# Kernel optimization log

Measured on AMD Instinct MI355X. Metric: run time of the kernel, lower is better.

The kernel has to match this reference:

```python
import jax, jax.numpy as jnp
import numpy as np

N_NODES = 100000
N_EDGES = 1600000
NUM_RELS = 200
NUM_BASES = 4
IN_FEAT = 20   # hardcoded by `view(-1, 1, 20)` in the torch source
OUT_FEAT = 20
SUBMAT_IN = IN_FEAT // NUM_BASES   # 5
SUBMAT_OUT = OUT_FEAT // NUM_BASES # 5


def setup_inputs() -> dict:
    key = jax.random.key(0)
    ks = jax.random.split(key, 9)
    return {
        "h": jax.random.normal(ks[0], (N_NODES, IN_FEAT), dtype=jnp.float32),
        "weight": jax.random.normal(ks[1], (NUM_RELS, NUM_BASES * SUBMAT_IN * SUBMAT_OUT), dtype=jnp.float32),
        "bias_term": jax.random.normal(ks[2], (NUM_RELS, OUT_FEAT), dtype=jnp.float32),
        "gate_weight": jax.random.normal(ks[3], (NUM_RELS, OUT_FEAT, 1), dtype=jnp.float32),
        "gate_bias": jax.random.normal(ks[4], (NUM_RELS, 1), dtype=jnp.float32),
        "loop_weight": jax.random.normal(ks[5], (IN_FEAT, OUT_FEAT), dtype=jnp.float32),
        "edge_src": jax.random.randint(ks[6], (N_EDGES,), 0, N_NODES, dtype=jnp.int32),
        "edge_dst": jax.random.randint(ks[7], (N_EDGES,), 0, N_NODES, dtype=jnp.int32),
        "etype": jax.random.randint(ks[8], (NUM_RELS,), 0, NUM_RELS, dtype=jnp.int32) if False else jax.random.randint(ks[8], (N_EDGES,), 0, NUM_RELS, dtype=jnp.int32),
    }


def reference(h, weight, bias_term, gate_weight, gate_bias, loop_weight, edge_src, edge_dst, etype):
    n_nodes = h.shape[0]
    # self-loop message (dropout=0.0 -> identity)
    loop_message = h @ loop_weight                                    # [N, out]
    # per-edge relation-indexed gathers
    W = weight[etype].reshape(-1, NUM_BASES, SUBMAT_IN, SUBMAT_OUT)   # [E, B, si, so]
    src = h[edge_src]                                                 # [E, in]
    node = src.reshape(-1, NUM_BASES, SUBMAT_IN)                      # [E, B, si]
    # block-diagonal small matmul
    msg = jnp.einsum('ebi,ebio->ebo', node, W).reshape(-1, OUT_FEAT)  # [E, out]
    # gate: sigmoid(<full src node, gate_weight_r> + gate_bias_r)
    gw = gate_weight[etype, :, 0]                                     # [E, out(=20=in)]
    gb = gate_bias[etype, 0]                                          # [E]
    gate = jax.nn.sigmoid(jnp.sum(src * gw, axis=-1) + gb)            # [E]
    msg = gate[:, None] * (msg + bias_term[etype])                    # [E, out]
    # scatter-sum aggregation to destination nodes (zero init for isolated nodes)
    agg = jax.ops.segment_sum(msg, edge_dst, num_segments=n_nodes)    # [N, out]
    return jax.nn.relu(agg + loop_message)
```

## Files before the change

kernel.cpp:

```cpp
#include <hip/hip_runtime.h>
#include <hip/hip_fp16.h>
#include <math.h>

#define IN_FEAT 20
#define OUT_FEAT 20
#define NUM_BASES 4
#define SUBMAT_IN 5
#define SUBMAT_OUT 5
#define NUM_RELS 200
#define CAP 64
#define NPB 160
#define BCAP 3072


__global__ void zero_kernel(int* __restrict__ p, int n) {
    int i = blockIdx.x * blockDim.x + threadIdx.x;
    if (i < n) p[i] = 0;
}

__global__ void __launch_bounds__(1024)
bucket_scatter_kernel(const int* __restrict__ edge_src,
                      const int* __restrict__ edge_dst,
                      const int* __restrict__ etype,
                      int* __restrict__ cursor,
                      int2* __restrict__ bucketed,
                      int n_edges, int nb) {
    __shared__ int lhist[1024];
    __shared__ int lbase[1024];
    __shared__ int lrank[1024];
    int tid = threadIdx.x;
    for (int i = tid; i < nb; i += 1024) { lhist[i] = 0; lrank[i] = 0; }
    __syncthreads();

    int e0 = blockIdx.x * 4096 + tid * 4;
    int s[4], d[4], t[4], bk[4];
    bool val[4];
    if (e0 + 3 < n_edges) {
        int4 sv = *(const int4*)(edge_src + e0);
        int4 dv = *(const int4*)(edge_dst + e0);
        int4 tv = *(const int4*)(etype + e0);
        s[0]=sv.x; s[1]=sv.y; s[2]=sv.z; s[3]=sv.w;
        d[0]=dv.x; d[1]=dv.y; d[2]=dv.z; d[3]=dv.w;
        t[0]=tv.x; t[1]=tv.y; t[2]=tv.z; t[3]=tv.w;
        val[0]=val[1]=val[2]=val[3]=true;
    } else {
#pragma unroll
        for (int k = 0; k < 4; ++k) {
            int e = e0 + k;
            val[k] = (e < n_edges);
            s[k] = val[k] ? edge_src[e] : 0;
            d[k] = val[k] ? edge_dst[e] : 0;
            t[k] = val[k] ? etype[e] : 0;
        }
    }
#pragma unroll
    for (int k = 0; k < 4; ++k) {
        bk[k] = d[k] / NPB;
        if (val[k]) atomicAdd(&lhist[bk[k]], 1);
    }
    __syncthreads();
    for (int i = tid; i < nb; i += 1024)
        if (lhist[i] > 0) lbase[i] = atomicAdd(&cursor[i], lhist[i]);
    __syncthreads();
#pragma unroll
    for (int k = 0; k < 4; ++k) {
        if (val[k]) {
            int r = atomicAdd(&lrank[bk[k]], 1);
            int off = lbase[bk[k]] + r;
            if (off < BCAP) {
                unsigned packed = (unsigned)s[k] | ((unsigned)t[k] << 17);
                bucketed[(size_t)bk[k] * BCAP + off] = make_int2(d[k], (int)packed);
            }
        }
    }
}

__global__ void __launch_bounds__(1024)
bucket_scan_kernel(const int* __restrict__ cursor, int* __restrict__ bucket_base,
                   int nb) {
    __shared__ int s[1024];
    int tid = threadIdx.x;
    int v = (tid < nb) ? min(cursor[tid], BCAP) : 0;
    s[tid] = v;
    __syncthreads();
    for (int step = 1; step < 1024; step <<= 1) {
        int t = (tid >= step) ? s[tid - step] : 0;
        __syncthreads();
        if (tid >= step) s[tid] += t;
        __syncthreads();
    }
    if (tid < nb) bucket_base[tid] = s[tid] - v;
}

__global__ void __launch_bounds__(1024)
place_csr_kernel(const int* __restrict__ cursor,
                 const int* __restrict__ bucket_base,
                 const int2* __restrict__ bucketed,
                 unsigned* __restrict__ records,
                 int* __restrict__ cnt,
                 int* __restrict__ off,
                 int n_nodes) {
    __shared__ int lcnt[NPB];
    __shared__ int sscan[NPB];
    __shared__ int lrank[NPB];
    int b = blockIdx.x, tid = threadIdx.x;
    int node0 = b * NPB;
    if (tid < NPB) { lcnt[tid] = 0; lrank[tid] = 0; }
    __syncthreads();
    int m = cursor[b]; if (m > BCAP) m = BCAP;
    int gbase = bucket_base[b];

    for (int i = tid; i < m; i += 1024) {
        int2 r = bucketed[(size_t)b * BCAP + i];
        atomicAdd(&lcnt[r.x - node0], 1);
    }
    __syncthreads();
    if (tid < NPB) sscan[tid] = lcnt[tid];
    __syncthreads();
    for (int step = 1; step < NPB; step <<= 1) {
        int t = (tid < NPB && tid >= step) ? sscan[tid - step] : 0;
        __syncthreads();
        if (tid < NPB && tid >= step) sscan[tid] += t;
        __syncthreads();
    }
    if (tid < NPB) {
        int excl = sscan[tid] - lcnt[tid];
        int v = node0 + tid;
        if (v < n_nodes) { cnt[v] = lcnt[tid]; off[v] = gbase + excl; }
        sscan[tid] = excl;
    }
    __syncthreads();
    for (int i = tid; i < m; i += 1024) {
        int2 r = bucketed[(size_t)b * BCAP + i];
        int dl = r.x - node0;
        int rk = atomicAdd(&lrank[dl], 1);
        records[(size_t)gbase + sscan[dl] + rk] = (unsigned)r.y;
    }
}

__global__ void __launch_bounds__(256)
hpad_kernel(const float* __restrict__ h, __half* __restrict__ h_pad, int n_nodes) {
    int v = blockIdx.x * 256 + threadIdx.x;
    if (v >= n_nodes) return;
    const float4* hp = (const float4*)(h + (size_t)v * IN_FEAT);
    float4 a = hp[0], b = hp[1], c = hp[2], d = hp[3], e = hp[4];
    __half2 p0 = __floats2half2_rn(a.x, a.y), p1 = __floats2half2_rn(a.z, a.w);
    __half2 p2 = __floats2half2_rn(b.x, b.y), p3 = __floats2half2_rn(b.z, b.w);
    __half2 p4 = __floats2half2_rn(c.x, c.y), p5 = __floats2half2_rn(c.z, c.w);
    __half2 p6 = __floats2half2_rn(d.x, d.y), p7 = __floats2half2_rn(d.z, d.w);
    __half2 p8 = __floats2half2_rn(e.x, e.y), p9 = __floats2half2_rn(e.z, e.w);
    uint4 w0, w1; uint2 w2;
    w0.x = *(unsigned*)&p0; w0.y = *(unsigned*)&p1; w0.z = *(unsigned*)&p2; w0.w = *(unsigned*)&p3;
    w1.x = *(unsigned*)&p4; w1.y = *(unsigned*)&p5; w1.z = *(unsigned*)&p6; w1.w = *(unsigned*)&p7;
    w2.x = *(unsigned*)&p8; w2.y = *(unsigned*)&p9;
    char* dst = (char*)(h_pad + (size_t)v * 32);
    *(uint4*)(dst)      = w0;
    *(uint4*)(dst + 16) = w1;
    *(uint2*)(dst + 32) = w2;
}

__global__ void __launch_bounds__(1024, 4)
gather_kernel(const float* __restrict__ h,
              const __half* __restrict__ h_pad,
              const float* __restrict__ loop_weight,
              const float* __restrict__ weight,
              const float* __restrict__ bias_term,
              const float* __restrict__ gate_weight,
              const float* __restrict__ gate_bias,
              const int* __restrict__ cnt,
              const int* __restrict__ off,
              const unsigned* __restrict__ records,
              float* __restrict__ out, int n_nodes, int n_groups) {
    __shared__ __half2 lds_wp[NUM_RELS * 51];
    __shared__ float   lds_gwt[IN_FEAT * NUM_RELS];
    __shared__ float   lds_gb[NUM_RELS];
    __shared__ float   lds_lw[IN_FEAT * OUT_FEAT];
    int tid = threadIdx.x;
    for (int idx = tid; idx < NUM_RELS * 50; idx += 1024) {
        int t = idx / 50, f = idx - t * 50;
        lds_wp[t * 51 + f] = __floats2half2_rn(weight[t * 100 + f],
                                               weight[t * 100 + f + 50]);
    }
    for (int idx = tid; idx < IN_FEAT * NUM_RELS; idx += 1024) {
        int t = idx / IN_FEAT, i = idx - t * IN_FEAT;
        lds_gwt[i * NUM_RELS + t] = gate_weight[idx];
    }
    for (int idx = tid; idx < NUM_RELS; idx += 1024) lds_gb[idx] = gate_bias[idx];
    for (int idx = tid; idx < IN_FEAT * OUT_FEAT; idx += 1024) lds_lw[idx] = loop_weight[idx];
    __syncthreads();

    int wave = blockIdx.x * 16 + (tid >> 6);
    int nwaves = gridDim.x * 16;
    int l = tid & 63;
    int l16 = l & 15;

    for (int grp = wave; grp < n_groups; grp += nwaves) {
        int v = grp * 4 + (l >> 4);
        bool valid = (v < n_nodes);
        int c = 0, base = 0;
        if (valid) { c = cnt[v]; base = off[v]; }
        if (c > CAP) c = CAP;

        float acc[OUT_FEAT];
#pragma unroll
        for (int j = 0; j < OUT_FEAT; ++j) acc[j] = 0.0f;

        if (valid) {
#pragma unroll
            for (int i0 = 0; i0 < 2; ++i0) {
                int i = l16 + i0 * 16;
                if (i < IN_FEAT) {
                    float s = h[(size_t)v * IN_FEAT + i];
#pragma unroll
                    for (int j = 0; j < OUT_FEAT; ++j)
                        acc[j] = fmaf(s, lds_lw[i * OUT_FEAT + j], acc[j]);
                }
            }
        }

#pragma unroll
        for (int it = 0; it < 4; ++it) {
            int slot = l16 + it * 16;
            if (valid && slot < c) {
                unsigned p = records[(size_t)base + slot];
                int srcid = (int)(p & 0x1FFFFu);
                int t = (int)(p >> 17);

                const char* sp = (const char*)(h_pad + (size_t)srcid * 32);
                uint4 A = *(const uint4*)(sp);
                uint4 B = *(const uint4*)(sp + 16);
                uint2 C = *(const uint2*)(sp + 32);
                float src[IN_FEAT];
                {
                    unsigned u[10] = {A.x, A.y, A.z, A.w, B.x, B.y, B.z, B.w, C.x, C.y};
#pragma unroll
                    for (int q = 0; q < 10; ++q) {
                        __half2 hv = *reinterpret_cast<__half2*>(&u[q]);
                        float2 f = __half22float2(hv);
                        src[2 * q] = f.x; src[2 * q + 1] = f.y;
                    }
                }

                float g = lds_gb[t];
#pragma unroll
                for (int i = 0; i < IN_FEAT; ++i)
                    g = fmaf(src[i], lds_gwt[i * NUM_RELS + t], g);
                g = 1.0f / (1.0f + __expf(-g));

#pragma unroll
                for (int i = 0; i < IN_FEAT; ++i) src[i] *= g;

                const __half2* wp = lds_wp + t * 51;
#pragma unroll
                for (int f = 0; f < 50; ++f) {
                    float2 w = __half22float2(wp[f]);
                    const int b0 = f / 25, r = f - b0 * 25;
                    const int i0 = r / 5, o0 = r - i0 * 5;
                    acc[b0 * 5 + o0] =
                        fmaf(src[b0 * 5 + i0], w.x, acc[b0 * 5 + o0]);
                    acc[(b0 + 2) * 5 + o0] =
                        fmaf(src[(b0 + 2) * 5 + i0], w.y, acc[(b0 + 2) * 5 + o0]);
                }

                const float4* btp = (const float4*)(bias_term + (size_t)t * OUT_FEAT);
#pragma unroll
                for (int k = 0; k < OUT_FEAT / 4; ++k) {
                    float4 bv = btp[k];
                    acc[4 * k + 0] = fmaf(g, bv.x, acc[4 * k + 0]);
                    acc[4 * k + 1] = fmaf(g, bv.y, acc[4 * k + 1]);
                    acc[4 * k + 2] = fmaf(g, bv.z, acc[4 * k + 2]);
                    acc[4 * k + 3] = fmaf(g, bv.w, acc[4 * k + 3]);
                }
            }
        }

#pragma unroll
        for (int mask = 8; mask > 0; mask >>= 1) {
#pragma unroll
            for (int j = 0; j < OUT_FEAT; ++j)
                acc[j] += __shfl_xor(acc[j], mask, 16);
        }

        if (valid && l16 < OUT_FEAT / 4) {
            float4 tv;
            tv.x = fmaxf(acc[4 * l16 + 0], 0.0f);
            tv.y = fmaxf(acc[4 * l16 + 1], 0.0f);
            tv.z = fmaxf(acc[4 * l16 + 2], 0.0f);
            tv.w = fmaxf(acc[4 * l16 + 3], 0.0f);
            ((float4*)(out + (size_t)v * OUT_FEAT))[l16] = tv;
        }
    }
}

__global__ void loop_msg_kernel(const float* __restrict__ h,
                                const float* __restrict__ loop_weight,
                                float* __restrict__ out, int n_nodes) {
    int v = blockIdx.x * blockDim.x + threadIdx.x;
    if (v >= n_nodes) return;
    float src[IN_FEAT];
    const float4* hp = (const float4*)(h + (size_t)v * IN_FEAT);
#pragma unroll
    for (int i = 0; i < IN_FEAT / 4; ++i) {
        float4 t = hp[i];
        src[4 * i + 0] = t.x; src[4 * i + 1] = t.y;
        src[4 * i + 2] = t.z; src[4 * i + 3] = t.w;
    }
    float acc[OUT_FEAT];
#pragma unroll
    for (int j = 0; j < OUT_FEAT; ++j) acc[j] = 0.0f;
#pragma unroll
    for (int i = 0; i < IN_FEAT; ++i) {
        float s = src[i];
#pragma unroll
        for (int j = 0; j < OUT_FEAT; ++j)
            acc[j] = fmaf(s, loop_weight[i * OUT_FEAT + j], acc[j]);
    }
    float4* op = (float4*)(out + (size_t)v * OUT_FEAT);
#pragma unroll
    for (int j = 0; j < OUT_FEAT / 4; ++j) {
        float4 t;
        t.x = acc[4 * j + 0]; t.y = acc[4 * j + 1];
        t.z = acc[4 * j + 2]; t.w = acc[4 * j + 3];
        op[j] = t;
    }
}

__global__ void edge_atomic_kernel(const float* __restrict__ h,
                                   const float* __restrict__ weight,
                                   const float* __restrict__ bias_term,
                                   const float* __restrict__ gate_weight,
                                   const float* __restrict__ gate_bias,
                                   const int* __restrict__ edge_src,
                                   const int* __restrict__ edge_dst,
                                   const int* __restrict__ etype,
                                   float* __restrict__ out, int n_edges) {
    int e = blockIdx.x * blockDim.x + threadIdx.x;
    if (e >= n_edges) return;
    int s = edge_src[e], d = edge_dst[e], t = etype[e];
    float src[IN_FEAT];
    const float4* hp = (const float4*)(h + (size_t)s * IN_FEAT);
#pragma unroll
    for (int i = 0; i < IN_FEAT / 4; ++i) {
        float4 v = hp[i];
        src[4 * i + 0] = v.x; src[4 * i + 1] = v.y;
        src[4 * i + 2] = v.z; src[4 * i + 3] = v.w;
    }
    const float* W = weight + (size_t)t * 100;
    float msg[OUT_FEAT];
#pragma unroll
    for (int j = 0; j < OUT_FEAT; ++j) msg[j] = 0.0f;
#pragma unroll
    for (int b = 0; b < NUM_BASES; ++b)
#pragma unroll
        for (int i = 0; i < SUBMAT_IN; ++i) {
            float sv = src[b * SUBMAT_IN + i];
#pragma unroll
            for (int o = 0; o < SUBMAT_OUT; ++o)
                msg[b * SUBMAT_OUT + o] =
                    fmaf(sv, W[(b * SUBMAT_IN + i) * SUBMAT_OUT + o],
                         msg[b * SUBMAT_OUT + o]);
        }
    const float* gw = gate_weight + (size_t)t * OUT_FEAT;
    float g = gate_bias[t];
#pragma unroll
    for (int i = 0; i < IN_FEAT; ++i) g = fmaf(src[i], gw[i], g);
    g = 1.0f / (1.0f + __expf(-g));
    const float* bt = bias_term + (size_t)t * OUT_FEAT;
    float* dstp = out + (size_t)d * OUT_FEAT;
#pragma unroll
    for (int j = 0; j < OUT_FEAT; ++j) atomicAdd(&dstp[j], g * (msg[j] + bt[j]));
}

__global__ void relu_kernel(float* __restrict__ out, int n4) {
    int i = blockIdx.x * blockDim.x + threadIdx.x;
    if (i >= n4) return;
    float4* p = (float4*)out;
    float4 v = p[i];
    v.x = fmaxf(v.x, 0.0f); v.y = fmaxf(v.y, 0.0f);
    v.z = fmaxf(v.z, 0.0f); v.w = fmaxf(v.w, 0.0f);
    p[i] = v;
}

extern "C" void kernel_launch(void* const* d_in, const int* in_sizes, int n_in,
                              void* d_out, int out_size, void* d_ws, size_t ws_size,
                              hipStream_t stream) {
    const float* h           = (const float*)d_in[0];
    const float* weight      = (const float*)d_in[1];
    const float* bias_term   = (const float*)d_in[2];
    const float* gate_weight = (const float*)d_in[3];
    const float* gate_bias   = (const float*)d_in[4];
    const float* loop_weight = (const float*)d_in[5];
    const int* edge_src      = (const int*)d_in[6];
    const int* edge_dst      = (const int*)d_in[7];
    const int* etype         = (const int*)d_in[8];
    float* out = (float*)d_out;

    const int n_nodes = in_sizes[0] / IN_FEAT;
    const int n_edges = in_sizes[6];
    const int nb = (n_nodes + NPB - 1) / NPB;

    size_t off_cursor   = 0;
    size_t off_bbase    = (((size_t)nb * 4 + 127) / 128) * 128;
    size_t off_bucketed = ((off_bbase + (size_t)nb * 4 + 127) / 128) * 128;
    size_t off_records  = ((off_bucketed + (size_t)nb * BCAP * 8 + 127) / 128) * 128;
    size_t off_cnt      = ((off_records + (size_t)n_edges * 4 + 127) / 128) * 128;
    size_t off_offs     = ((off_cnt + (size_t)n_nodes * 4 + 127) / 128) * 128;
    size_t off_hpad     = ((off_offs + (size_t)n_nodes * 4 + 127) / 128) * 128;
    size_t need = off_hpad + (size_t)n_nodes * 64;

    bool ok = (ws_size >= need) && (n_nodes <= (1 << 17)) && (nb <= 1024) &&
              (in_sizes[4] == NUM_RELS) && (in_sizes[1] == NUM_RELS * 100) &&
              (in_sizes[5] == IN_FEAT * OUT_FEAT);

    if (ok) {
        int*  cursor      = (int*)((char*)d_ws + off_cursor);
        int*  bucket_base = (int*)((char*)d_ws + off_bbase);
        int2* bucketed    = (int2*)((char*)d_ws + off_bucketed);
        unsigned* records = (unsigned*)((char*)d_ws + off_records);
        int*  cnt         = (int*)((char*)d_ws + off_cnt);
        int*  off         = (int*)((char*)d_ws + off_offs);
        __half* h_pad     = (__half*)((char*)d_ws + off_hpad);

        zero_kernel<<<(nb + 255) / 256, 256, 0, stream>>>(cursor, nb);
        hpad_kernel<<<(n_nodes + 255) / 256, 256, 0, stream>>>(h, h_pad, n_nodes);
        bucket_scatter_kernel<<<(n_edges + 4095) / 4096, 1024, 0, stream>>>(
            edge_src, edge_dst, etype, cursor, bucketed, n_edges, nb);
        bucket_scan_kernel<<<1, 1024, 0, stream>>>(cursor, bucket_base, nb);
        place_csr_kernel<<<nb, 1024, 0, stream>>>(
            cursor, bucket_base, bucketed, records, cnt, off, n_nodes);
        int n_groups = (n_nodes + 3) / 4;
        gather_kernel<<<512, 1024, 0, stream>>>(
            h, h_pad, loop_weight, weight, bias_term, gate_weight, gate_bias,
            cnt, off, records, out, n_nodes, n_groups);
    } else {
        loop_msg_kernel<<<(n_nodes + 255) / 256, 256, 0, stream>>>(
            h, loop_weight, out, n_nodes);
        edge_atomic_kernel<<<(n_edges + 255) / 256, 256, 0, stream>>>(
            h, weight, bias_term, gate_weight, gate_bias,
            edge_src, edge_dst, etype, out, n_edges);
        relu_kernel<<<(n_nodes * OUT_FEAT / 4 + 255) / 256, 256, 0, stream>>>(
            out, n_nodes * OUT_FEAT / 4);
    }
}
```

Baseline: 205.9 us.

## Aggregate directly from destination buckets with LDS atomics, dropping CSR build

Removes the scan and CSR placement kernels and replaces the per-node gather with a per-bucket aggregation kernel. Each block processes one destination bucket's edges, accumulates messages into shared memory with float atomics, then adds the self-loop matmul and applies ReLU. It also folds cursor zeroing into the h_pad conversion kernel. This cuts two launches and the records/cnt/off traffic, at the cost of LDS atomic contention, nondeterministic summation order, and re-staging the relation tables in shared memory once per bucket block (about 625 blocks instead of 512).

```diff
diff --git a/kernel.cpp b/kernel.cpp
--- a/kernel.cpp
+++ b/kernel.cpp
@@ -8,139 +8,16 @@
 #define SUBMAT_IN 5
 #define SUBMAT_OUT 5
 #define NUM_RELS 200
-#define CAP 64
 #define NPB 160
 #define BCAP 3072
-
-
-__global__ void zero_kernel(int* __restrict__ p, int n) {
-    int i = blockIdx.x * blockDim.x + threadIdx.x;
-    if (i < n) p[i] = 0;
-}
-
-__global__ void __launch_bounds__(1024)
-bucket_scatter_kernel(const int* __restrict__ edge_src,
-                      const int* __restrict__ edge_dst,
-                      const int* __restrict__ etype,
-                      int* __restrict__ cursor,
-                      int2* __restrict__ bucketed,
-                      int n_edges, int nb) {
-    __shared__ int lhist[1024];
-    __shared__ int lbase[1024];
-    __shared__ int lrank[1024];
-    int tid = threadIdx.x;
-    for (int i = tid; i < nb; i += 1024) { lhist[i] = 0; lrank[i] = 0; }
-    __syncthreads();
-
-    int e0 = blockIdx.x * 4096 + tid * 4;
-    int s[4], d[4], t[4], bk[4];
-    bool val[4];
-    if (e0 + 3 < n_edges) {
-        int4 sv = *(const int4*)(edge_src + e0);
-        int4 dv = *(const int4*)(edge_dst + e0);
-        int4 tv = *(const int4*)(etype + e0);
-        s[0]=sv.x; s[1]=sv.y; s[2]=sv.z; s[3]=sv.w;
-        d[0]=dv.x; d[1]=dv.y; d[2]=dv.z; d[3]=dv.w;
-        t[0]=tv.x; t[1]=tv.y; t[2]=tv.z; t[3]=tv.w;
-        val[0]=val[1]=val[2]=val[3]=true;
-    } else {
-#pragma unroll
-        for (int k = 0; k < 4; ++k) {
-            int e = e0 + k;
-            val[k] = (e < n_edges);
-            s[k] = val[k] ? edge_src[e] : 0;
-            d[k] = val[k] ? edge_dst[e] : 0;
-            t[k] = val[k] ? etype[e] : 0;
-        }
-    }
-#pragma unroll
-    for (int k = 0; k < 4; ++k) {
-        bk[k] = d[k] / NPB;
-        if (val[k]) atomicAdd(&lhist[bk[k]], 1);
-    }
-    __syncthreads();
-    for (int i = tid; i < nb; i += 1024)
-        if (lhist[i] > 0) lbase[i] = atomicAdd(&cursor[i], lhist[i]);
-    __syncthreads();
-#pragma unroll
-    for (int k = 0; k < 4; ++k) {
-        if (val[k]) {
-            int r = atomicAdd(&lrank[bk[k]], 1);
-            int off = lbase[bk[k]] + r;
-            if (off < BCAP) {
-                unsigned packed = (unsigned)s[k] | ((unsigned)t[k] << 17);
-                bucketed[(size_t)bk[k] * BCAP + off] = make_int2(d[k], (int)packed);
-            }
-        }
-    }
-}
-
-__global__ void __launch_bounds__(1024)
-bucket_scan_kernel(const int* __restrict__ cursor, int* __restrict__ bucket_base,
-                   int nb) {
-    __shared__ int s[1024];
-    int tid = threadIdx.x;
-    int v = (tid < nb) ? min(cursor[tid], BCAP) : 0;
-    s[tid] = v;
-    __syncthreads();
-    for (int step = 1; step < 1024; step <<= 1) {
-        int t = (tid >= step) ? s[tid - step] : 0;
-        __syncthreads();
-        if (tid >= step) s[tid] += t;
-        __syncthreads();
-    }
-    if (tid < nb) bucket_base[tid] = s[tid] - v;
-}
-
-__global__ void __launch_bounds__(1024)
-place_csr_kernel(const int* __restrict__ cursor,
-                 const int* __restrict__ bucket_base,
-                 const int2* __restrict__ bucketed,
-                 unsigned* __restrict__ records,
-                 int* __restrict__ cnt,
-                 int* __restrict__ off,
-                 int n_nodes) {
-    __shared__ int lcnt[NPB];
-    __shared__ int sscan[NPB];
-    __shared__ int lrank[NPB];
-    int b = blockIdx.x, tid = threadIdx.x;
-    int node0 = b * NPB;
-    if (tid < NPB) { lcnt[tid] = 0; lrank[tid] = 0; }
-    __syncthreads();
-    int m = cursor[b]; if (m > BCAP) m = BCAP;
-    int gbase = bucket_base[b];
-
-    for (int i = tid; i < m; i += 1024) {
-        int2 r = bucketed[(size_t)b * BCAP + i];
-        atomicAdd(&lcnt[r.x - node0], 1);
-    }
-    __syncthreads();
-    if (tid < NPB) sscan[tid] = lcnt[tid];
-    __syncthreads();
-    for (int step = 1; step < NPB; step <<= 1) {
-        int t = (tid < NPB && tid >= step) ? sscan[tid - step] : 0;
-        __syncthreads();
-        if (tid < NPB && tid >= step) sscan[tid] += t;
-        __syncthreads();
-    }
-    if (tid < NPB) {
-        int excl = sscan[tid] - lcnt[tid];
-        int v = node0 + tid;
-        if (v < n_nodes) { cnt[v] = lcnt[tid]; off[v] = gbase + excl; }
-        sscan[tid] = excl;
-    }
-    __syncthreads();
-    for (int i = tid; i < m; i += 1024) {
-        int2 r = bucketed[(size_t)b * BCAP + i];
-        int dl = r.x - node0;
-        int rk = atomicAdd(&lrank[dl], 1);
-        records[(size_t)gbase + sscan[dl] + rk] = (unsigned)r.y;
-    }
-}
+#define ACCW 21
+
 
 __global__ void __launch_bounds__(256)
-hpad_kernel(const float* __restrict__ h, __half* __restrict__ h_pad, int n_nodes) {
+hpad_zero_kernel(const float* __restrict__ h, __half* __restrict__ h_pad,
+                 int* __restrict__ cursor, int n_nodes, int nb) {
     int v = blockIdx.x * 256 + threadIdx.x;
+    if (v < nb) cursor[v] = 0;
     if (v >= n_nodes) return;
     const float4* hp = (const float4*)(h + (size_t)v * IN_FEAT);
     float4 a = hp[0], b = hp[1], c = hp[2], d = hp[3], e = hp[4];
@@ -159,23 +36,83 @@
     *(uint2*)(dst + 32) = w2;
 }
 
+__global__ void __launch_bounds__(1024)
+bucket_scatter_kernel(const int* __restrict__ edge_src,
+                      const int* __restrict__ edge_dst,
+                      const int* __restrict__ etype,
+                      int* __restrict__ cursor,
+                      int2* __restrict__ bucketed,
+                      int n_edges, int nb) {
+    __shared__ int lhist[1024];
+    __shared__ int lbase[1024];
+    __shared__ int lrank[1024];
+    int tid = threadIdx.x;
+    for (int i = tid; i < nb; i += 1024) { lhist[i] = 0; lrank[i] = 0; }
+    __syncthreads();
+
+    int e0 = blockIdx.x * 4096 + tid * 4;
+    int s[4], d[4], t[4], bk[4];
+    bool val[4];
+    if (e0 + 3 < n_edges) {
+        int4 sv = *(const int4*)(edge_src + e0);
+        int4 dv = *(const int4*)(edge_dst + e0);
+        int4 tv = *(const int4*)(etype + e0);
+        s[0]=sv.x; s[1]=sv.y; s[2]=sv.z; s[3]=sv.w;
+        d[0]=dv.x; d[1]=dv.y; d[2]=dv.z; d[3]=dv.w;
+        t[0]=tv.x; t[1]=tv.y; t[2]=tv.z; t[3]=tv.w;
+        val[0]=val[1]=val[2]=val[3]=true;
+    } else {
+#pragma unroll
+        for (int k = 0; k < 4; ++k) {
+            int e = e0 + k;
+            val[k] = (e < n_edges);
+            s[k] = val[k] ? edge_src[e] : 0;
+            d[k] = val[k] ? edge_dst[e] : 0;
+            t[k] = val[k] ? etype[e] : 0;
+        }
+    }
+#pragma unroll
+    for (int k = 0; k < 4; ++k) {
+        bk[k] = d[k] / NPB;
+        if (val[k]) atomicAdd(&lhist[bk[k]], 1);
+    }
+    __syncthreads();
+    for (int i = tid; i < nb; i += 1024)
+        if (lhist[i] > 0) lbase[i] = atomicAdd(&cursor[i], lhist[i]);
+    __syncthreads();
+#pragma unroll
+    for (int k = 0; k < 4; ++k) {
+        if (val[k]) {
+            int r = atomicAdd(&lrank[bk[k]], 1);
+            int off = lbase[bk[k]] + r;
+            if (off < BCAP) {
+                unsigned packed = (unsigned)s[k] | ((unsigned)t[k] << 17);
+                bucketed[(size_t)bk[k] * BCAP + off] = make_int2(d[k], (int)packed);
+            }
+        }
+    }
+}
+
 __global__ void __launch_bounds__(1024, 4)
-gather_kernel(const float* __restrict__ h,
-              const __half* __restrict__ h_pad,
-              const float* __restrict__ loop_weight,
-              const float* __restrict__ weight,
-              const float* __restrict__ bias_term,
-              const float* __restrict__ gate_weight,
-              const float* __restrict__ gate_bias,
-              const int* __restrict__ cnt,
-              const int* __restrict__ off,
-              const unsigned* __restrict__ records,
-              float* __restrict__ out, int n_nodes, int n_groups) {
+bucket_aggregate_kernel(const float* __restrict__ h,
+                        const __half* __restrict__ h_pad,
+                        const float* __restrict__ loop_weight,
+                        const float* __restrict__ weight,
+                        const float* __restrict__ bias_term,
+                        const float* __restrict__ gate_weight,
+                        const float* __restrict__ gate_bias,
+                        const int* __restrict__ cursor,
+                        const int2* __restrict__ bucketed,
+                        float* __restrict__ out, int n_nodes) {
     __shared__ __half2 lds_wp[NUM_RELS * 51];
     __shared__ float   lds_gwt[IN_FEAT * NUM_RELS];
     __shared__ float   lds_gb[NUM_RELS];
     __shared__ float   lds_lw[IN_FEAT * OUT_FEAT];
+    __shared__ float   lds_acc[NPB * ACCW];
     int tid = threadIdx.x;
+    int b = blockIdx.x;
+    int node0 = b * NPB;
+
     for (int idx = tid; idx < NUM_RELS * 50; idx += 1024) {
         int t = idx / 50, f = idx - t * 50;
         lds_wp[t * 51 + f] = __floats2half2_rn(weight[t * 100 + f],
@@ -187,107 +124,79 @@
     }
     for (int idx = tid; idx < NUM_RELS; idx += 1024) lds_gb[idx] = gate_bias[idx];
     for (int idx = tid; idx < IN_FEAT * OUT_FEAT; idx += 1024) lds_lw[idx] = loop_weight[idx];
-    __syncthreads();
-
-    int wave = blockIdx.x * 16 + (tid >> 6);
-    int nwaves = gridDim.x * 16;
-    int l = tid & 63;
-    int l16 = l & 15;
-
-    for (int grp = wave; grp < n_groups; grp += nwaves) {
-        int v = grp * 4 + (l >> 4);
-        bool valid = (v < n_nodes);
-        int c = 0, base = 0;
-        if (valid) { c = cnt[v]; base = off[v]; }
-        if (c > CAP) c = CAP;
-
-        float acc[OUT_FEAT];
-#pragma unroll
-        for (int j = 0; j < OUT_FEAT; ++j) acc[j] = 0.0f;
-
-        if (valid) {
-#pragma unroll
-            for (int i0 = 0; i0 < 2; ++i0) {
-                int i = l16 + i0 * 16;
-                if (i < IN_FEAT) {
-                    float s = h[(size_t)v * IN_FEAT + i];
-#pragma unroll
-                    for (int j = 0; j < OUT_FEAT; ++j)
-                        acc[j] = fmaf(s, lds_lw[i * OUT_FEAT + j], acc[j]);
-                }
-            }
-        }
-
-#pragma unroll
-        for (int it = 0; it < 4; ++it) {
-            int slot = l16 + it * 16;
-            if (valid && slot < c) {
-                unsigned p = records[(size_t)base + slot];
-                int srcid = (int)(p & 0x1FFFFu);
-                int t = (int)(p >> 17);
-
-                const char* sp = (const char*)(h_pad + (size_t)srcid * 32);
-                uint4 A = *(const uint4*)(sp);
-                uint4 B = *(const uint4*)(sp + 16);
-                uint2 C = *(const uint2*)(sp + 32);
-                float src[IN_FEAT];
-                {
-                    unsigned u[10] = {A.x, A.y, A.z, A.w, B.x, B.y, B.z, B.w, C.x, C.y};
-#pragma unroll
-                    for (int q = 0; q < 10; ++q) {
-                        __half2 hv = *reinterpret_cast<__half2*>(&u[q]);
-                        float2 f = __half22float2(hv);
-                        src[2 * q] = f.x; src[2 * q + 1] = f.y;
-                    }
-                }
-
-                float g = lds_gb[t];
-#pragma unroll
-                for (int i = 0; i < IN_FEAT; ++i)
-                    g = fmaf(src[i], lds_gwt[i * NUM_RELS + t], g);
-                g = 1.0f / (1.0f + __expf(-g));
-
-#pragma unroll
-                for (int i = 0; i < IN_FEAT; ++i) src[i] *= g;
-
-                const __half2* wp = lds_wp + t * 51;
-#pragma unroll
-                for (int f = 0; f < 50; ++f) {
-                    float2 w = __half22float2(wp[f]);
-                    const int b0 = f / 25, r = f - b0 * 25;
-                    const int i0 = r / 5, o0 = r - i0 * 5;
-                    acc[b0 * 5 + o0] =
-                        fmaf(src[b0 * 5 + i0], w.x, acc[b0 * 5 + o0]);
-                    acc[(b0 + 2) * 5 + o0] =
-                        fmaf(src[(b0 + 2) * 5 + i0], w.y, acc[(b0 + 2) * 5 + o0]);
-                }
-
-                const float4* btp = (const float4*)(bias_term + (size_t)t * OUT_FEAT);
-#pragma unroll
-                for (int k = 0; k < OUT_FEAT / 4; ++k) {
-                    float4 bv = btp[k];
-                    acc[4 * k + 0] = fmaf(g, bv.x, acc[4 * k + 0]);
-                    acc[4 * k + 1] = fmaf(g, bv.y, acc[4 * k + 1]);
-                    acc[4 * k + 2] = fmaf(g, bv.z, acc[4 * k + 2]);
-                    acc[4 * k + 3] = fmaf(g, bv.w, acc[4 * k + 3]);
-                }
-            }
-        }
-
-#pragma unroll
-        for (int mask = 8; mask > 0; mask >>= 1) {
-#pragma unroll
-            for (int j = 0; j < OUT_FEAT; ++j)
-                acc[j] += __shfl_xor(acc[j], mask, 16);
-        }
-
-        if (valid && l16 < OUT_FEAT / 4) {
-            float4 tv;
-            tv.x = fmaxf(acc[4 * l16 + 0], 0.0f);
-            tv.y = fmaxf(acc[4 * l16 + 1], 0.0f);
-            tv.z = fmaxf(acc[4 * l16 + 2], 0.0f);
-            tv.w = fmaxf(acc[4 * l16 + 3], 0.0f);
-            ((float4*)(out + (size_t)v * OUT_FEAT))[l16] = tv;
+    for (int idx = tid; idx < NPB * ACCW; idx += 1024) lds_acc[idx] = 0.0f;
+    __syncthreads();
+
+    int m = cursor[b]; if (m > BCAP) m = BCAP;
+
+    for (int i = tid; i < m; i += 1024) {
+        int2 r = bucketed[(size_t)b * BCAP + i];
+        int dl = r.x - node0;
+        unsigned p = (unsigned)r.y;
+        int srcid = (int)(p & 0x1FFFFu);
+        int t = (int)(p >> 17);
+
+        const char* sp = (const char*)(h_pad + (size_t)srcid * 32);
+        uint4 A = *(const uint4*)(sp);
+        uint4 B = *(const uint4*)(sp + 16);
+        uint2 C = *(const uint2*)(sp + 32);
+        float src[IN_FEAT];
+        {
+            unsigned u0;
+            float2 f2;
+#define UNP(word, o) u0 = (word); f2 = __half22float2(*reinterpret_cast<__half2*>(&u0)); \
+                     src[(o)] = f2.x; src[(o) + 1] = f2.y;
+            UNP(A.x, 0)  UNP(A.y, 2)  UNP(A.z, 4)  UNP(A.w, 6)
+            UNP(B.x, 8)  UNP(B.y, 10) UNP(B.z, 12) UNP(B.w, 14)
+            UNP(C.x, 16) UNP(C.y, 18)
+#undef UNP
+        }
+
+        float g = lds_gb[t];
+#pragma unroll
+        for (int i2 = 0; i2 < IN_FEAT; ++i2)
+            g = fmaf(src[i2], lds_gwt[i2 * NUM_RELS + t], g);
+        g = 1.0f / (1.0f + __expf(-g));
+
+#pragma unroll
+        for (int i2 = 0; i2 < IN_FEAT; ++i2) src[i2] *= g;
+
+        float msg[OUT_FEAT];
+        const float4* btp = (const float4*)(bias_term + (size_t)t * OUT_FEAT);
+#pragma unroll
+        for (int k = 0; k < OUT_FEAT / 4; ++k) {
+            float4 bv = btp[k];
+            msg[4 * k + 0] = g * bv.x; msg[4 * k + 1] = g * bv.y;
+            msg[4 * k + 2] = g * bv.z; msg[4 * k + 3] = g * bv.w;
+        }
+
+        const __half2* wp = lds_wp + t * 51;
+#pragma unroll
+        for (int f = 0; f < 50; ++f) {
+            float2 w = __half22float2(wp[f]);
+            const int b0 = f / 25, rr = f - b0 * 25;
+            const int i0 = rr / 5, o0 = rr - i0 * 5;
+            msg[b0 * 5 + o0] = fmaf(src[b0 * 5 + i0], w.x, msg[b0 * 5 + o0]);
+            msg[(b0 + 2) * 5 + o0] = fmaf(src[(b0 + 2) * 5 + i0], w.y, msg[(b0 + 2) * 5 + o0]);
+        }
+
+        float* accp = lds_acc + dl * ACCW;
+#pragma unroll
+        for (int j = 0; j < OUT_FEAT; ++j)
+            atomicAdd(&accp[j], msg[j]);
+    }
+    __syncthreads();
+
+    for (int task = tid; task < NPB * OUT_FEAT; task += 1024) {
+        int vl = task / OUT_FEAT, j = task - vl * OUT_FEAT;
+        int v = node0 + vl;
+        if (v < n_nodes) {
+            const float* hv = h + (size_t)v * IN_FEAT;
+            float s = lds_acc[vl * ACCW + j];
+#pragma unroll
+            for (int i2 = 0; i2 < IN_FEAT; ++i2)
+                s = fmaf(hv[i2], lds_lw[i2 * OUT_FEAT + j], s);
+            out[(size_t)v * OUT_FEAT + j] = fmaxf(s, 0.0f);
         }
     }
 }
@@ -400,12 +309,8 @@
     const int nb = (n_nodes + NPB - 1) / NPB;
 
     size_t off_cursor   = 0;
-    size_t off_bbase    = (((size_t)nb * 4 + 127) / 128) * 128;
-    size_t off_bucketed = ((off_bbase + (size_t)nb * 4 + 127) / 128) * 128;
-    size_t off_records  = ((off_bucketed + (size_t)nb * BCAP * 8 + 127) / 128) * 128;
-    size_t off_cnt      = ((off_records + (size_t)n_edges * 4 + 127) / 128) * 128;
-    size_t off_offs     = ((off_cnt + (size_t)n_nodes * 4 + 127) / 128) * 128;
-    size_t off_hpad     = ((off_offs + (size_t)n_nodes * 4 + 127) / 128) * 128;
+    size_t off_bucketed = (((size_t)nb * 4 + 127) / 128) * 128;
+    size_t off_hpad     = ((off_bucketed + (size_t)nb * BCAP * 8 + 127) / 128) * 128;
     size_t need = off_hpad + (size_t)n_nodes * 64;
 
     bool ok = (ws_size >= need) && (n_nodes <= (1 << 17)) && (nb <= 1024) &&
@@ -414,24 +319,16 @@
 
     if (ok) {
         int*  cursor      = (int*)((char*)d_ws + off_cursor);
-        int*  bucket_base = (int*)((char*)d_ws + off_bbase);
         int2* bucketed    = (int2*)((char*)d_ws + off_bucketed);
-        unsigned* records = (unsigned*)((char*)d_ws + off_records);
-        int*  cnt         = (int*)((char*)d_ws + off_cnt);
-        int*  off         = (int*)((char*)d_ws + off_offs);
         __half* h_pad     = (__half*)((char*)d_ws + off_hpad);
 
-        zero_kernel<<<(nb + 255) / 256, 256, 0, stream>>>(cursor, nb);
-        hpad_kernel<<<(n_nodes + 255) / 256, 256, 0, stream>>>(h, h_pad, n_nodes);
+        hpad_zero_kernel<<<(n_nodes + 255) / 256, 256, 0, stream>>>(
+            h, h_pad, cursor, n_nodes, nb);
         bucket_scatter_kernel<<<(n_edges + 4095) / 4096, 1024, 0, stream>>>(
             edge_src, edge_dst, etype, cursor, bucketed, n_edges, nb);
-        bucket_scan_kernel<<<1, 1024, 0, stream>>>(cursor, bucket_base, nb);
-        place_csr_kernel<<<nb, 1024, 0, stream>>>(
-            cursor, bucket_base, bucketed, records, cnt, off, n_nodes);
-        int n_groups = (n_nodes + 3) / 4;
-        gather_kernel<<<512, 1024, 0, stream>>>(
+        bucket_aggregate_kernel<<<nb, 1024, 0, stream>>>(
             h, h_pad, loop_weight, weight, bias_term, gate_weight, gate_bias,
-            cnt, off, records, out, n_nodes, n_groups);
+            cursor, bucketed, out, n_nodes);
     } else {
         loop_msg_kernel<<<(n_nodes + 255) / 256, 256, 0, stream>>>(
             h, loop_weight, out, n_nodes);
```

Measured after the change: 347.5 us. 68.7% more time.

## Fuse CSR placement into gather kernel using per-bucket LDS records

Applied to the files above, without the earlier changes.

Removes the global bucket scan and place_csr kernels. Each gather block now owns one bucket of 160 destination nodes: it counts and scans edges in LDS, places the records in LDS, and then aggregates. The zero-init is also folded into the hpad kernel. This drops two launches and a global round trip of the records, cnt and off arrays. In exchange every one of the ~625 blocks reloads the relation weight tables into LDS and uses more shared memory, which may lower occupancy.

```diff
diff --git a/kernel.cpp b/kernel.cpp
--- a/kernel.cpp
+++ b/kernel.cpp
@@ -11,136 +11,14 @@
 #define CAP 64
 #define NPB 160
 #define BCAP 3072
-
-
-__global__ void zero_kernel(int* __restrict__ p, int n) {
-    int i = blockIdx.x * blockDim.x + threadIdx.x;
-    if (i < n) p[i] = 0;
-}
-
-__global__ void __launch_bounds__(1024)
-bucket_scatter_kernel(const int* __restrict__ edge_src,
-                      const int* __restrict__ edge_dst,
-                      const int* __restrict__ etype,
-                      int* __restrict__ cursor,
-                      int2* __restrict__ bucketed,
-                      int n_edges, int nb) {
-    __shared__ int lhist[1024];
-    __shared__ int lbase[1024];
-    __shared__ int lrank[1024];
-    int tid = threadIdx.x;
-    for (int i = tid; i < nb; i += 1024) { lhist[i] = 0; lrank[i] = 0; }
-    __syncthreads();
-
-    int e0 = blockIdx.x * 4096 + tid * 4;
-    int s[4], d[4], t[4], bk[4];
-    bool val[4];
-    if (e0 + 3 < n_edges) {
-        int4 sv = *(const int4*)(edge_src + e0);
-        int4 dv = *(const int4*)(edge_dst + e0);
-        int4 tv = *(const int4*)(etype + e0);
-        s[0]=sv.x; s[1]=sv.y; s[2]=sv.z; s[3]=sv.w;
-        d[0]=dv.x; d[1]=dv.y; d[2]=dv.z; d[3]=dv.w;
-        t[0]=tv.x; t[1]=tv.y; t[2]=tv.z; t[3]=tv.w;
-        val[0]=val[1]=val[2]=val[3]=true;
-    } else {
-#pragma unroll
-        for (int k = 0; k < 4; ++k) {
-            int e = e0 + k;
-            val[k] = (e < n_edges);
-            s[k] = val[k] ? edge_src[e] : 0;
-            d[k] = val[k] ? edge_dst[e] : 0;
-            t[k] = val[k] ? etype[e] : 0;
-        }
-    }
-#pragma unroll
-    for (int k = 0; k < 4; ++k) {
-        bk[k] = d[k] / NPB;
-        if (val[k]) atomicAdd(&lhist[bk[k]], 1);
-    }
-    __syncthreads();
-    for (int i = tid; i < nb; i += 1024)
-        if (lhist[i] > 0) lbase[i] = atomicAdd(&cursor[i], lhist[i]);
-    __syncthreads();
-#pragma unroll
-    for (int k = 0; k < 4; ++k) {
-        if (val[k]) {
-            int r = atomicAdd(&lrank[bk[k]], 1);
-            int off = lbase[bk[k]] + r;
-            if (off < BCAP) {
-                unsigned packed = (unsigned)s[k] | ((unsigned)t[k] << 17);
-                bucketed[(size_t)bk[k] * BCAP + off] = make_int2(d[k], (int)packed);
-            }
-        }
-    }
-}
-
-__global__ void __launch_bounds__(1024)
-bucket_scan_kernel(const int* __restrict__ cursor, int* __restrict__ bucket_base,
-                   int nb) {
-    __shared__ int s[1024];
-    int tid = threadIdx.x;
-    int v = (tid < nb) ? min(cursor[tid], BCAP) : 0;
-    s[tid] = v;
-    __syncthreads();
-    for (int step = 1; step < 1024; step <<= 1) {
-        int t = (tid >= step) ? s[tid - step] : 0;
-        __syncthreads();
-        if (tid >= step) s[tid] += t;
-        __syncthreads();
-    }
-    if (tid < nb) bucket_base[tid] = s[tid] - v;
-}
-
-__global__ void __launch_bounds__(1024)
-place_csr_kernel(const int* __restrict__ cursor,
-                 const int* __restrict__ bucket_base,
-                 const int2* __restrict__ bucketed,
-                 unsigned* __restrict__ records,
-                 int* __restrict__ cnt,
-                 int* __restrict__ off,
-                 int n_nodes) {
-    __shared__ int lcnt[NPB];
-    __shared__ int sscan[NPB];
-    __shared__ int lrank[NPB];
-    int b = blockIdx.x, tid = threadIdx.x;
-    int node0 = b * NPB;
-    if (tid < NPB) { lcnt[tid] = 0; lrank[tid] = 0; }
-    __syncthreads();
-    int m = cursor[b]; if (m > BCAP) m = BCAP;
-    int gbase = bucket_base[b];
-
-    for (int i = tid; i < m; i += 1024) {
-        int2 r = bucketed[(size_t)b * BCAP + i];
-        atomicAdd(&lcnt[r.x - node0], 1);
-    }
-    __syncthreads();
-    if (tid < NPB) sscan[tid] = lcnt[tid];
-    __syncthreads();
-    for (int step = 1; step < NPB; step <<= 1) {
-        int t = (tid < NPB && tid >= step) ? sscan[tid - step] : 0;
-        __syncthreads();
-        if (tid < NPB && tid >= step) sscan[tid] += t;
-        __syncthreads();
-    }
-    if (tid < NPB) {
-        int excl = sscan[tid] - lcnt[tid];
-        int v = node0 + tid;
-        if (v < n_nodes) { cnt[v] = lcnt[tid]; off[v] = gbase + excl; }
-        sscan[tid] = excl;
-    }
-    __syncthreads();
-    for (int i = tid; i < m; i += 1024) {
-        int2 r = bucketed[(size_t)b * BCAP + i];
-        int dl = r.x - node0;
-        int rk = atomicAdd(&lrank[dl], 1);
-        records[(size_t)gbase + sscan[dl] + rk] = (unsigned)r.y;
-    }
-}
+#define NPASS ((NPB + 63) / 64)
+
 
 __global__ void __launch_bounds__(256)
-hpad_kernel(const float* __restrict__ h, __half* __restrict__ h_pad, int n_nodes) {
+hpad_zero_kernel(const float* __restrict__ h, __half* __restrict__ h_pad,
+                 int* __restrict__ cursor, int n_nodes, int nb) {
     int v = blockIdx.x * 256 + threadIdx.x;
+    if (v < nb) cursor[v] = 0;
     if (v >= n_nodes) return;
     const float4* hp = (const float4*)(h + (size_t)v * IN_FEAT);
     float4 a = hp[0], b = hp[1], c = hp[2], d = hp[3], e = hp[4];
@@ -159,23 +37,86 @@
     *(uint2*)(dst + 32) = w2;
 }
 
+__global__ void __launch_bounds__(1024)
+bucket_scatter_kernel(const int* __restrict__ edge_src,
+                      const int* __restrict__ edge_dst,
+                      const int* __restrict__ etype,
+                      int* __restrict__ cursor,
+                      int2* __restrict__ bucketed,
+                      int n_edges, int nb) {
+    __shared__ int lhist[1024];
+    __shared__ int lbase[1024];
+    __shared__ int lrank[1024];
+    int tid = threadIdx.x;
+    for (int i = tid; i < nb; i += 1024) { lhist[i] = 0; lrank[i] = 0; }
+    __syncthreads();
+
+    int e0 = blockIdx.x * 4096 + tid * 4;
+    int s[4], d[4], t[4], bk[4];
+    bool val[4];
+    if (e0 + 3 < n_edges) {
+        int4 sv = *(const int4*)(edge_src + e0);
+        int4 dv = *(const int4*)(edge_dst + e0);
+        int4 tv = *(const int4*)(etype + e0);
+        s[0]=sv.x; s[1]=sv.y; s[2]=sv.z; s[3]=sv.w;
+        d[0]=dv.x; d[1]=dv.y; d[2]=dv.z; d[3]=dv.w;
+        t[0]=tv.x; t[1]=tv.y; t[2]=tv.z; t[3]=tv.w;
+        val[0]=val[1]=val[2]=val[3]=true;
+    } else {
+#pragma unroll
+        for (int k = 0; k < 4; ++k) {
+            int e = e0 + k;
+            val[k] = (e < n_edges);
+            s[k] = val[k] ? edge_src[e] : 0;
+            d[k] = val[k] ? edge_dst[e] : 0;
+            t[k] = val[k] ? etype[e] : 0;
+        }
+    }
+#pragma unroll
+    for (int k = 0; k < 4; ++k) {
+        bk[k] = d[k] / NPB;
+        if (val[k]) atomicAdd(&lhist[bk[k]], 1);
+    }
+    __syncthreads();
+    for (int i = tid; i < nb; i += 1024)
+        if (lhist[i] > 0) lbase[i] = atomicAdd(&cursor[i], lhist[i]);
+    __syncthreads();
+#pragma unroll
+    for (int k = 0; k < 4; ++k) {
+        if (val[k]) {
+            int r = atomicAdd(&lrank[bk[k]], 1);
+            int off = lbase[bk[k]] + r;
+            if (off < BCAP) {
+                unsigned packed = (unsigned)s[k] | ((unsigned)t[k] << 17);
+                bucketed[(size_t)bk[k] * BCAP + off] = make_int2(d[k], (int)packed);
+            }
+        }
+    }
+}
+
 __global__ void __launch_bounds__(1024, 4)
-gather_kernel(const float* __restrict__ h,
-              const __half* __restrict__ h_pad,
-              const float* __restrict__ loop_weight,
-              const float* __restrict__ weight,
-              const float* __restrict__ bias_term,
-              const float* __restrict__ gate_weight,
-              const float* __restrict__ gate_bias,
-              const int* __restrict__ cnt,
-              const int* __restrict__ off,
-              const unsigned* __restrict__ records,
-              float* __restrict__ out, int n_nodes, int n_groups) {
-    __shared__ __half2 lds_wp[NUM_RELS * 51];
-    __shared__ float   lds_gwt[IN_FEAT * NUM_RELS];
-    __shared__ float   lds_gb[NUM_RELS];
-    __shared__ float   lds_lw[IN_FEAT * OUT_FEAT];
+bucket_gather_kernel(const float* __restrict__ h,
+                     const __half* __restrict__ h_pad,
+                     const float* __restrict__ loop_weight,
+                     const float* __restrict__ weight,
+                     const float* __restrict__ bias_term,
+                     const float* __restrict__ gate_weight,
+                     const float* __restrict__ gate_bias,
+                     const int* __restrict__ cursor,
+                     const int2* __restrict__ bucketed,
+                     float* __restrict__ out, int n_nodes) {
+    __shared__ __half2  lds_wp[NUM_RELS * 51];
+    __shared__ float    lds_gwt[IN_FEAT * NUM_RELS];
+    __shared__ float    lds_gb[NUM_RELS];
+    __shared__ float    lds_lw[IN_FEAT * OUT_FEAT];
+    __shared__ unsigned lds_rec[BCAP];
+    __shared__ int      lcnt[NPB];
+    __shared__ int      loff[NPB];
+    __shared__ int      lrank[NPB];
     int tid = threadIdx.x;
+    int b = blockIdx.x;
+    int node0 = b * NPB;
+
     for (int idx = tid; idx < NUM_RELS * 50; idx += 1024) {
         int t = idx / 50, f = idx - t * 50;
         lds_wp[t * 51 + f] = __floats2half2_rn(weight[t * 100 + f],
@@ -187,19 +128,47 @@
     }
     for (int idx = tid; idx < NUM_RELS; idx += 1024) lds_gb[idx] = gate_bias[idx];
     for (int idx = tid; idx < IN_FEAT * OUT_FEAT; idx += 1024) lds_lw[idx] = loop_weight[idx];
-    __syncthreads();
-
-    int wave = blockIdx.x * 16 + (tid >> 6);
-    int nwaves = gridDim.x * 16;
+    if (tid < NPB) { lcnt[tid] = 0; lrank[tid] = 0; }
+    __syncthreads();
+
+    int m = cursor[b]; if (m > BCAP) m = BCAP;
+
+    for (int i = tid; i < m; i += 1024) {
+        int2 r = bucketed[(size_t)b * BCAP + i];
+        atomicAdd(&lcnt[r.x - node0], 1);
+    }
+    __syncthreads();
+    if (tid < NPB) loff[tid] = lcnt[tid];
+    __syncthreads();
+    for (int step = 1; step < NPB; step <<= 1) {
+        int t = (tid < NPB && tid >= step) ? loff[tid - step] : 0;
+        __syncthreads();
+        if (tid < NPB && tid >= step) loff[tid] += t;
+        __syncthreads();
+    }
+    if (tid < NPB) loff[tid] -= lcnt[tid];
+    __syncthreads();
+    for (int i = tid; i < m; i += 1024) {
+        int2 r = bucketed[(size_t)b * BCAP + i];
+        int dl = r.x - node0;
+        int rk = atomicAdd(&lrank[dl], 1);
+        lds_rec[loff[dl] + rk] = (unsigned)r.y;
+    }
+    __syncthreads();
+
+    int wave = tid >> 6;
     int l = tid & 63;
     int l16 = l & 15;
-
-    for (int grp = wave; grp < n_groups; grp += nwaves) {
-        int v = grp * 4 + (l >> 4);
-        bool valid = (v < n_nodes);
-        int c = 0, base = 0;
-        if (valid) { c = cnt[v]; base = off[v]; }
+    int sub = l >> 4;
+
+#pragma unroll
+    for (int pass = 0; pass < NPASS; ++pass) {
+        int vl = pass * 64 + wave * 4 + sub;
+        int v = node0 + vl;
+        bool valid = (vl < NPB) && (v < n_nodes);
+        int c = valid ? lcnt[vl] : 0;
         if (c > CAP) c = CAP;
+        int base = valid ? loff[vl] : 0;
 
         float acc[OUT_FEAT];
 #pragma unroll
@@ -222,7 +191,7 @@
         for (int it = 0; it < 4; ++it) {
             int slot = l16 + it * 16;
             if (valid && slot < c) {
-                unsigned p = records[(size_t)base + slot];
+                unsigned p = lds_rec[base + slot];
                 int srcid = (int)(p & 0x1FFFFu);
                 int t = (int)(p >> 17);
 
@@ -400,12 +369,8 @@
     const int nb = (n_nodes + NPB - 1) / NPB;
 
     size_t off_cursor   = 0;
-    size_t off_bbase    = (((size_t)nb * 4 + 127) / 128) * 128;
-    size_t off_bucketed = ((off_bbase + (size_t)nb * 4 + 127) / 128) * 128;
-    size_t off_records  = ((off_bucketed + (size_t)nb * BCAP * 8 + 127) / 128) * 128;
-    size_t off_cnt      = ((off_records + (size_t)n_edges * 4 + 127) / 128) * 128;
-    size_t off_offs     = ((off_cnt + (size_t)n_nodes * 4 + 127) / 128) * 128;
-    size_t off_hpad     = ((off_offs + (size_t)n_nodes * 4 + 127) / 128) * 128;
+    size_t off_bucketed = (((size_t)nb * 4 + 127) / 128) * 128;
+    size_t off_hpad     = ((off_bucketed + (size_t)nb * BCAP * 8 + 127) / 128) * 128;
     size_t need = off_hpad + (size_t)n_nodes * 64;
 
     bool ok = (ws_size >= need) && (n_nodes <= (1 << 17)) && (nb <= 1024) &&
@@ -414,24 +379,16 @@
 
     if (ok) {
         int*  cursor      = (int*)((char*)d_ws + off_cursor);
-        int*  bucket_base = (int*)((char*)d_ws + off_bbase);
         int2* bucketed    = (int2*)((char*)d_ws + off_bucketed);
-        unsigned* records = (unsigned*)((char*)d_ws + off_records);
-        int*  cnt         = (int*)((char*)d_ws + off_cnt);
-        int*  off         = (int*)((char*)d_ws + off_offs);
         __half* h_pad     = (__half*)((char*)d_ws + off_hpad);
 
-        zero_kernel<<<(nb + 255) / 256, 256, 0, stream>>>(cursor, nb);
-        hpad_kernel<<<(n_nodes + 255) / 256, 256, 0, stream>>>(h, h_pad, n_nodes);
+        hpad_zero_kernel<<<(n_nodes + 255) / 256, 256, 0, stream>>>(
+            h, h_pad, cursor, n_nodes, nb);
         bucket_scatter_kernel<<<(n_edges + 4095) / 4096, 1024, 0, stream>>>(
             edge_src, edge_dst, etype, cursor, bucketed, n_edges, nb);
-        bucket_scan_kernel<<<1, 1024, 0, stream>>>(cursor, bucket_base, nb);
-        place_csr_kernel<<<nb, 1024, 0, stream>>>(
-            cursor, bucket_base, bucketed, records, cnt, off, n_nodes);
-        int n_groups = (n_nodes + 3) / 4;
-        gather_kernel<<<512, 1024, 0, stream>>>(
+        bucket_gather_kernel<<<nb, 1024, 0, stream>>>(
             h, h_pad, loop_weight, weight, bias_term, gate_weight, gate_bias,
-            cnt, off, records, out, n_nodes, n_groups);
+            cursor, bucketed, out, n_nodes);
     } else {
         loop_msg_kernel<<<(n_nodes + 255) / 256, 256, 0, stream>>>(
             h, loop_weight, out, n_nodes);
```

Measured after the change: 224.6 us. 1.09x slower.
